# Kernel optimization log

Measured on AMD Instinct MI355X. Metric: run time of the kernel, lower is better.

The kernel has to match this reference:

```python
import jax, jax.numpy as jnp
import numpy as np

EMB_DIM, D_H, BSZ, SEQ = 2048, 128, 4, 4096
HALF = D_H // 2


def apply_rope(x, sin, cos):
    # x: [b, s, d]; sin/cos: [s, d//2]; interleaved-pair rotation
    b, s, d = x.shape
    xr = x.reshape(b, s, d // 2, 2)
    x0, x1 = xr[..., 0], xr[..., 1]
    r0 = x0 * cos - x1 * sin
    r1 = x1 * cos + x0 * sin
    return jnp.stack([r0, r1], axis=-1).reshape(b, s, d)


def setup_inputs() -> dict:
    key = jax.random.key(0)
    kx, kq, kk, kv = jax.random.split(key, 4)
    x = jax.random.normal(kx, (BSZ, SEQ, EMB_DIM), dtype=jnp.float32)
    # causal mask (1 = attend, 0 = masked), matching mask[q,:] slicing in source
    mask = jnp.tril(jnp.ones((SEQ, SEQ), dtype=jnp.int32))
    # standard RoPE angle tables: [seq, d_h//2]
    inv_freq = 1.0 / (10000.0 ** (jnp.arange(HALF, dtype=jnp.float32) / HALF))
    angles = jnp.arange(SEQ, dtype=jnp.float32)[:, None] * inv_freq[None, :]
    sin, cos = jnp.sin(angles), jnp.cos(angles)
    scale = 1.0 / np.sqrt(EMB_DIM)
    W_Q = jax.random.normal(kq, (EMB_DIM, D_H), dtype=jnp.float32) * scale
    W_K = jax.random.normal(kk, (EMB_DIM, D_H), dtype=jnp.float32) * scale
    W_V = jax.random.normal(kv, (EMB_DIM, D_H), dtype=jnp.float32) * scale
    return {"x": x, "mask": mask, "sin": sin, "cos": cos,
            "W_Q": W_Q, "W_K": W_K, "W_V": W_V}


def reference(x, mask, sin, cos, W_Q, W_V, W_K):
    # QKV projections
    Q = apply_rope(x @ W_Q, sin, cos)  # [b, s, d_h]
    K = apply_rope(x @ W_K, sin, cos)  # [b, s, d_h]
    V = x @ W_V                        # [b, s, d_h]
    # The source's chunked loop is exactly full masked attention over all K/V.
    scores = jnp.einsum('bqd,bkd->bqk', Q, K) / jnp.sqrt(jnp.float32(D_H))
    scores = jnp.where(mask[None, :, :] == 0, -jnp.inf, scores)
    attn = jax.nn.softmax(scores, axis=-1)
    return jnp.einsum('bqk,bkd->bqd', attn, V)
```

## Files before the change

### kernel.cpp

```cpp
#include <hip/hip_runtime.h>
#include <stdint.h>
#include <stddef.h>

typedef __bf16 bf16;
typedef __bf16 bf16x8 __attribute__((ext_vector_type(8)));
typedef float f32x4 __attribute__((ext_vector_type(4)));
typedef unsigned int uint32x2 __attribute__((ext_vector_type(2)));
typedef unsigned int uint32x4 __attribute__((ext_vector_type(4)));

typedef const __attribute__((address_space(1))) uint32_t GU32;
typedef __attribute__((address_space(3))) uint32_t LU32;

__device__ __forceinline__ f32x4 mfma16(bf16x8 a, bf16x8 b, f32x4 c) {
  return __builtin_amdgcn_mfma_f32_16x16x32_bf16(a, b, c, 0, 0, 0);
}
__device__ __forceinline__ void gload16(const void* g, void* l) {
  __builtin_amdgcn_global_load_lds((GU32*)g, (LU32*)l, 16, 0, 0);
}

__global__ __launch_bounds__(256) void k_prep(const float* __restrict__ Wq,
                                              const float* __restrict__ Wk,
                                              const float* __restrict__ Wv,
                                              bf16* __restrict__ Wct) {
  __shared__ float tile[64][65];
  const int tid = threadIdx.x;
  const int widx = blockIdx.x >> 6, rem = blockIdx.x & 63;
  const int k0 = (rem >> 1) * 64, n0 = (rem & 1) * 64;
  const float* W = (widx == 0) ? Wq : (widx == 1) ? Wk : Wv;
  const int rg = tid >> 4, cq = tid & 15;
#pragma unroll
  for (int i = 0; i < 4; ++i) {
    int krow = i * 16 + rg;
    f32x4 v = *(const f32x4*)(W + (size_t)(k0 + krow) * 128 + n0 + cq * 4);
#pragma unroll
    for (int j = 0; j < 4; ++j) tile[krow][cq * 4 + j] = v[j];
  }
  __syncthreads();
#pragma unroll
  for (int i = 0; i < 4; ++i) {
    int nrow = i * 16 + rg;
    union { bf16 h[4]; uint32x2 u; } pk;
#pragma unroll
    for (int j = 0; j < 4; ++j) pk.h[j] = (bf16)tile[cq * 4 + j][nrow];
    *(uint32x2*)(Wct + (size_t)(widx * 128 + n0 + nrow) * 2048 + k0 + cq * 4) = pk.u;
  }
}

__global__ __launch_bounds__(256, 2) void k_proj(
    const float* __restrict__ x, const float* __restrict__ sint, const float* __restrict__ cost,
    const bf16* __restrict__ Wct, bf16* __restrict__ Qg, bf16* __restrict__ Kg,
    bf16* __restrict__ Vtg) {
  __shared__ __align__(16) uint8_t smem[65536];
  const int tid = threadIdx.x;
  const int lane = tid & 63, w = tid >> 6;
  const int l15 = lane & 15, l16 = lane >> 4;
  const int logical = (blockIdx.x & 7) * 64 + (blockIdx.x >> 3);
  const int nb = logical & 1, mb = logical >> 1;
  const int wm = w >> 1, wn = w & 1;
  const int arow = tid >> 2, aj = tid & 3;

  f32x4 acc[2][6] = {};
  f32x4 regA[4], regB[4];

  const float* abase = x + (size_t)(mb * 64 + arow) * 2048 + aj * 16;

  auto stageB = [&](int buf, int ks) {
    uint8_t* bbm = smem + buf * 32768 + 8192;
    int k0 = ks * 64;
#pragma unroll
    for (int i = 0; i < 6; ++i) {
      int L = i * 4096 + tid * 16;
      int n = L >> 7, cp = (L >> 4) & 7;
      int cc = cp ^ (n & 7);
      const uint8_t* src = (const uint8_t*)Wct + (((size_t)(nb * 192 + n) * 2048 + k0 + cc * 8) << 1);
      gload16(src, bbm + i * 4096 + w * 1024);
    }
  };
  auto loadA = [&](int ks, f32x4* r) {
    const f32x4* p = (const f32x4*)(abase + ks * 64);
#pragma unroll
    for (int i = 0; i < 4; ++i) r[i] = p[i];
  };
  auto writeA = [&](int buf, const f32x4* r) {
    uint8_t* ab = smem + buf * 32768;
#pragma unroll
    for (int h = 0; h < 2; ++h) {
      union { bf16 v[8]; uint32x4 u; } pk;
#pragma unroll
      for (int e = 0; e < 8; ++e) pk.v[e] = (bf16)r[h * 2 + (e >> 2)][e & 3];
      int c = aj * 2 + h;
      *(uint32x4*)(ab + arow * 128 + (((c ^ (arow & 7)) & 7) << 4)) = pk.u;
    }
  };
  auto compute = [&](int buf) {
    uint8_t* ab = smem + buf * 32768;
    uint8_t* bbm = ab + 8192;
    bf16x8 af[2][2], bv[2][6];
#pragma unroll
    for (int kk = 0; kk < 2; ++kk) {
#pragma unroll
      for (int mt = 0; mt < 2; ++mt) {
        int ml = wm * 32 + mt * 16 + l15;
        af[kk][mt] = *(const bf16x8*)(ab + ml * 128 + (((kk * 4 + l16) ^ (ml & 7)) << 4));
      }
#pragma unroll
      for (int nt = 0; nt < 6; ++nt) {
        int nl = wn * 96 + nt * 16 + l15;
        bv[kk][nt] = *(const bf16x8*)(bbm + nl * 128 + (((kk * 4 + l16) ^ (nl & 7)) << 4));
      }
    }
    __builtin_amdgcn_s_setprio(1);
#pragma unroll
    for (int kk = 0; kk < 2; ++kk)
#pragma unroll
      for (int mt = 0; mt < 2; ++mt)
#pragma unroll
        for (int nt = 0; nt < 6; ++nt)
          acc[mt][nt] = mfma16(af[kk][mt], bv[kk][nt], acc[mt][nt]);
    __builtin_amdgcn_s_setprio(0);
  };

  loadA(0, regA);
  stageB(0, 0);
  loadA(1, regB);
  writeA(0, regA);
  asm volatile("s_waitcnt vmcnt(4)" ::: "memory");
  asm volatile("s_waitcnt lgkmcnt(0)" ::: "memory");
  __builtin_amdgcn_s_barrier();

  for (int ks = 0; ks < 30; ks += 2) {
    {
      stageB(1, ks + 1);
      loadA(ks + 2, regA);
      compute(0);
      writeA(1, regB);
      asm volatile("s_waitcnt vmcnt(4)" ::: "memory");
      asm volatile("s_waitcnt lgkmcnt(0)" ::: "memory");
      __builtin_amdgcn_s_barrier();
    }
    {
      stageB(0, ks + 2);
      loadA(ks + 3, regB);
      compute(1);
      writeA(0, regA);
      asm volatile("s_waitcnt vmcnt(4)" ::: "memory");
      asm volatile("s_waitcnt lgkmcnt(0)" ::: "memory");
      __builtin_amdgcn_s_barrier();
    }
  }
  {
    stageB(1, 31);
    compute(0);
    writeA(1, regB);
    asm volatile("s_waitcnt vmcnt(0)" ::: "memory");
    asm volatile("s_waitcnt lgkmcnt(0)" ::: "memory");
    __builtin_amdgcn_s_barrier();
  }
  compute(1);

#pragma unroll
  for (int mt = 0; mt < 2; ++mt) {
    int gm = mb * 64 + wm * 32 + mt * 16 + l16 * 4;
    int bb = gm >> 12, s0 = gm & 4095;
#pragma unroll
    for (int nt = 0; nt < 6; ++nt) {
      int jcol = nb * 192 + wn * 96 + nt * 16 + l15;
      f32x4 v = acc[mt][nt];
      if (jcol < 256) {
        int p = (jcol & 127) >> 1;
        bool even = ((jcol & 1) == 0);
#pragma unroll
        for (int r = 0; r < 4; ++r) {
          float pv = __shfl_xor(v[r], 1);
          int s = s0 + r;
          float cs = cost[s * 64 + p], sn = sint[s * 64 + p];
          float nv = even ? (v[r] * cs - pv * sn) : (v[r] * cs + pv * sn);
          bf16 hb = (bf16)nv;
          if (jcol < 128) Qg[((size_t)(bb << 12) + s) * 128 + jcol] = hb;
          else            Kg[((size_t)(bb << 12) + s) * 128 + jcol - 128] = hb;
        }
      } else {
        int d = jcol - 256;
        union { bf16 h[4]; uint32x2 u; } pk;
#pragma unroll
        for (int r = 0; r < 4; ++r) pk.h[r] = (bf16)v[r];
        *(uint32x2*)((uint8_t*)Vtg + (((size_t)(bb << 7) + d) * 4096 + s0) * 2) = pk.u;
      }
    }
  }
}

__global__ __launch_bounds__(256, 2) void k_attn(
    const bf16* __restrict__ Qg, const bf16* __restrict__ Kg, const bf16* __restrict__ Vtg,
    float* __restrict__ PO, float* __restrict__ ML) {
  __shared__ __align__(16) uint8_t smem[81920];
  const int tid = threadIdx.x;
  const int lane = tid & 63, w = tid >> 6;
  const int l15 = lane & 15, l16 = lane >> 4;

  int gid = blockIdx.x;
  int b = gid / 80, rr = gid % 80;
  int j, c;
  if (rr < 8)       { j = rr;                 c = 0; }
  else if (rr < 24) { j = 8 + ((rr - 8) >> 1);  c = (rr - 8) & 1; }
  else if (rr < 48) { j = 16 + (rr - 24) / 3;   c = (rr - 24) % 3; }
  else              { j = 24 + ((rr - 48) >> 2); c = (rr - 48) & 3; }

  const int q0w = j * 128 + w * 32;
  const int kv_lo = c * 1024;
  const int kv_hi = min((c + 1) * 1024, (j + 1) * 128);
  const int T = (kv_hi - kv_lo) >> 6;

  bf16x8 qf[2][4];
#pragma unroll
  for (int qt = 0; qt < 2; ++qt)
#pragma unroll
    for (int kk = 0; kk < 4; ++kk)
      qf[qt][kk] = *(const bf16x8*)(Qg + ((size_t)(b << 12) + q0w + qt * 16 + l15) * 128 + kk * 32 + l16 * 8);

  f32x4 o[2][8] = {};
  float m_r[2] = {-1e30f, -1e30f};
  float l_r[2] = {0.f, 0.f};
  uint8_t* pb = smem + 65536 + w * 4096;

  auto stage = [&](int t) {
    uint8_t* kb = smem + (t & 1) * 32768;
    uint8_t* vb = kb + 16384;
    int kv0 = kv_lo + t * 64;
#pragma unroll
    for (int i = 0; i < 4; ++i) {
      int L = i * 4096 + tid * 16;
      {
        int kv = L >> 8, cp = (L >> 4) & 15, cc = cp ^ (kv & 7);
        const uint8_t* src = (const uint8_t*)Kg + ((size_t)((b << 12) + kv0 + kv) << 8) + (cc << 4);
        gload16(src, kb + i * 4096 + w * 1024);
      }
      {
        int d = L >> 7, cp = (L >> 4) & 7, cc = cp ^ (d & 7);
        const uint8_t* src = (const uint8_t*)Vtg + ((size_t)(((b << 7) + d) << 12) + kv0 + (cc << 3)) * 2;
        gload16(src, vb + i * 4096 + w * 1024);
      }
    }
  };

  stage(0);
  __syncthreads();

  for (int t = 0; t < T; ++t) {
    if (t + 1 < T) stage(t + 1);
    const int kv0 = kv_lo + t * 64;
    if (kv0 <= q0w + 31) {
      uint8_t* kb = smem + (t & 1) * 32768;
      uint8_t* vb = kb + 16384;
      f32x4 sfr[4][2] = {};
#pragma unroll
      for (int kk = 0; kk < 4; ++kk) {
#pragma unroll
        for (int kvt = 0; kvt < 4; ++kvt) {
          int kvl = kvt * 16 + l15;
          bf16x8 kf = *(const bf16x8*)(kb + (kvl << 8) + (((kk * 4 + l16) ^ (kvl & 7)) << 4));
#pragma unroll
          for (int qt = 0; qt < 2; ++qt)
            sfr[kvt][qt] = mfma16(kf, qf[qt][kk], sfr[kvt][qt]);
        }
      }
      const bool need_mask = (kv0 + 63 > q0w);
      const float scale = 0.08838834764831845f;
#pragma unroll
      for (int qt = 0; qt < 2; ++qt) {
        const int q = q0w + qt * 16 + l15;
        float pvv[4][4];
        float tmax = -1e30f;
#pragma unroll
        for (int kvt = 0; kvt < 4; ++kvt)
#pragma unroll
          for (int r = 0; r < 4; ++r) {
            float sv = sfr[kvt][qt][r] * scale;
            if (need_mask) {
              int kv = kv0 + kvt * 16 + l16 * 4 + r;
              if (kv > q) sv = -1e30f;
            }
            pvv[kvt][r] = sv;
            tmax = fmaxf(tmax, sv);
          }
        tmax = fmaxf(tmax, __shfl_xor(tmax, 16));
        tmax = fmaxf(tmax, __shfl_xor(tmax, 32));
        float mnew = fmaxf(m_r[qt], tmax);
        float corr = __expf(m_r[qt] - mnew);
        m_r[qt] = mnew;
        float rs = 0.f;
#pragma unroll
        for (int kvt = 0; kvt < 4; ++kvt)
#pragma unroll
          for (int r = 0; r < 4; ++r) {
            float p = __expf(pvv[kvt][r] - mnew);
            pvv[kvt][r] = p;
            rs += p;
          }
        rs += __shfl_xor(rs, 16);
        rs += __shfl_xor(rs, 32);
        l_r[qt] = l_r[qt] * corr + rs;
        const int qrow = qt * 16 + l15;
#pragma unroll
        for (int kvt = 0; kvt < 4; ++kvt) {
          union { bf16 h[4]; uint32x2 u; } pk;
#pragma unroll
          for (int r = 0; r < 4; ++r) pk.h[r] = (bf16)pvv[kvt][r];
          int kv2 = kvt * 32 + l16 * 8;
          *(uint32x2*)(pb + qrow * 128 + ((((kv2 >> 4) ^ (qrow & 7)) << 4) | (kv2 & 15))) = pk.u;
        }
#pragma unroll
        for (int r = 0; r < 4; ++r) {
          float cr = __shfl(corr, l16 * 4 + r);
#pragma unroll
          for (int dt = 0; dt < 8; ++dt) o[qt][dt][r] *= cr;
        }
      }
#pragma unroll
      for (int kvb = 0; kvb < 2; ++kvb) {
        bf16x8 pa[2];
#pragma unroll
        for (int qt = 0; qt < 2; ++qt) {
          int qrow = qt * 16 + l15;
          int kv2 = kvb * 64 + l16 * 16;
          pa[qt] = *(const bf16x8*)(pb + qrow * 128 + (((kv2 >> 4) ^ (qrow & 7)) << 4));
        }
#pragma unroll
        for (int dt = 0; dt < 8; ++dt) {
          int d = dt * 16 + l15;
          bf16x8 vf = *(const bf16x8*)(vb + (d << 7) + (((kvb * 4 + l16) ^ (d & 7)) << 4));
#pragma unroll
          for (int qt = 0; qt < 2; ++qt)
            o[qt][dt] = mfma16(pa[qt], vf, o[qt][dt]);
        }
      }
    }
    __syncthreads();
  }

  float* POb = PO + (size_t)((b * 32 + j) * 4 + c) * 16384;
#pragma unroll
  for (int qt = 0; qt < 2; ++qt)
#pragma unroll
    for (int dt = 0; dt < 8; ++dt)
#pragma unroll
      for (int r = 0; r < 4; ++r)
        POb[(w * 32 + qt * 16 + l16 * 4 + r) * 128 + dt * 16 + l15] = o[qt][dt][r];
  float* MLb = ML + (size_t)((b * 32 + j) * 4 + c) * 256;
  if (l16 == 0) {
#pragma unroll
    for (int qt = 0; qt < 2; ++qt) {
      MLb[w * 32 + qt * 16 + l15] = m_r[qt];
      MLb[128 + w * 32 + qt * 16 + l15] = l_r[qt];
    }
  }
}

__global__ void k_combine(const float* __restrict__ PO, const float* __restrict__ ML,
                          float* __restrict__ out) {
  int blk = blockIdx.x;
  int b = blk >> 5, j = blk & 31;
  int nc = 1 + (j >> 3);
  int t = threadIdx.x;
  int q = t >> 1, half = t & 1;
  const float* MLb = ML + (size_t)(b * 32 + j) * 4 * 256;
  float mv[4], lv[4];
  float ms = -1e30f;
  for (int cc = 0; cc < nc; ++cc) {
    mv[cc] = MLb[cc * 256 + q];
    lv[cc] = MLb[cc * 256 + 128 + q];
    ms = fmaxf(ms, mv[cc]);
  }
  float wgt[4];
  float den = 0.f;
  for (int cc = 0; cc < nc; ++cc) { wgt[cc] = __expf(mv[cc] - ms); den += wgt[cc] * lv[cc]; }
  float inv = 1.f / den;
  const float* POb = PO + (size_t)(b * 32 + j) * 4 * 16384 + q * 128 + half * 64;
  float* ob = out + ((size_t)(b << 12) + j * 128 + q) * 128 + half * 64;
  for (int d = 0; d < 64; d += 4) {
    f32x4 a = {0.f, 0.f, 0.f, 0.f};
    for (int cc = 0; cc < nc; ++cc) {
      f32x4 v = *(const f32x4*)(POb + cc * 16384 + d);
      a += v * wgt[cc];
    }
    a *= inv;
    *(f32x4*)(ob + d) = a;
  }
}

extern "C" void kernel_launch(void* const* d_in, const int* in_sizes, int n_in,
                              void* d_out, int out_size, void* d_ws, size_t ws_size,
                              hipStream_t stream) {
  const float* x = (const float*)d_in[0];
  const float* sint = (const float*)d_in[2];
  const float* cost = (const float*)d_in[3];
  const float* Wq = (const float*)d_in[4];
  const float* Wk = (const float*)d_in[5];
  const float* Wv = (const float*)d_in[6];
  uint8_t* ws = (uint8_t*)d_ws;

  bf16* Wct = (bf16*)(ws + 0x0);
  bf16* Qg  = (bf16*)(ws + 0x180000);
  bf16* Kg  = (bf16*)(ws + 0x580000);
  bf16* Vtg = (bf16*)(ws + 0x980000);
  float* PO = (float*)(ws + 0xD80000);
  float* ML = (float*)(ws + 0x2D80000);
  float* out = (float*)d_out;

  hipLaunchKernelGGL(k_prep, dim3(192), dim3(256), 0, stream, Wq, Wk, Wv, Wct);
  hipLaunchKernelGGL(k_proj, dim3(512), dim3(256), 0, stream, x, sint, cost, Wct, Qg, Kg, Vtg);
  hipLaunchKernelGGL(k_attn, dim3(320), dim3(256), 0, stream, Qg, Kg, Vtg, PO, ML);
  hipLaunchKernelGGL(k_combine, dim3(128), dim3(256), 0, stream, PO, ML, out);
}
```

Before: 132.2 us.

## Give each projection block the full 384-column output so x is read once

The projection kernel now uses 512-thread blocks, each covering 64 rows across all 384 Q/K/V columns. Before, two blocks split the columns and each read and converted the same x tile. Each of the 8 waves owns 48 columns over all 64 rows, and LDS grows to 112 KB so only one block fits per CU. The aim is to halve the global reads of fp32 x, at the cost of fewer blocks (256), lower occupancy, and more B-tile LDS traffic per block.

```diff
diff --git a/kernel.cpp b/kernel.cpp
--- a/kernel.cpp
+++ b/kernel.cpp
@@ -46,66 +46,60 @@
   }
 }
 
-__global__ __launch_bounds__(256, 2) void k_proj(
+__global__ __launch_bounds__(512, 1) void k_proj(
     const float* __restrict__ x, const float* __restrict__ sint, const float* __restrict__ cost,
     const bf16* __restrict__ Wct, bf16* __restrict__ Qg, bf16* __restrict__ Kg,
     bf16* __restrict__ Vtg) {
-  __shared__ __align__(16) uint8_t smem[65536];
+  __shared__ __align__(16) uint8_t smem[114688];
   const int tid = threadIdx.x;
   const int lane = tid & 63, w = tid >> 6;
   const int l15 = lane & 15, l16 = lane >> 4;
-  const int logical = (blockIdx.x & 7) * 64 + (blockIdx.x >> 3);
-  const int nb = logical & 1, mb = logical >> 1;
-  const int wm = w >> 1, wn = w & 1;
-  const int arow = tid >> 2, aj = tid & 3;
-
-  f32x4 acc[2][6] = {};
-  f32x4 regA[4], regB[4];
-
-  const float* abase = x + (size_t)(mb * 64 + arow) * 2048 + aj * 16;
+  const int mb = blockIdx.x;
+  const int arow = tid >> 3, aj = tid & 7;
+
+  f32x4 acc[4][3] = {};
+  f32x4 regA[2], regB[2];
+
+  const float* abase = x + (size_t)(mb * 64 + arow) * 2048 + aj * 8;
 
   auto stageB = [&](int buf, int ks) {
-    uint8_t* bbm = smem + buf * 32768 + 8192;
+    uint8_t* bbm = smem + 16384 + buf * 49152;
     int k0 = ks * 64;
 #pragma unroll
     for (int i = 0; i < 6; ++i) {
-      int L = i * 4096 + tid * 16;
+      int L = i * 8192 + tid * 16;
       int n = L >> 7, cp = (L >> 4) & 7;
       int cc = cp ^ (n & 7);
-      const uint8_t* src = (const uint8_t*)Wct + (((size_t)(nb * 192 + n) * 2048 + k0 + cc * 8) << 1);
-      gload16(src, bbm + i * 4096 + w * 1024);
+      const uint8_t* src = (const uint8_t*)Wct + (((size_t)n * 2048 + k0 + cc * 8) << 1);
+      gload16(src, bbm + i * 8192 + w * 1024);
     }
   };
   auto loadA = [&](int ks, f32x4* r) {
     const f32x4* p = (const f32x4*)(abase + ks * 64);
-#pragma unroll
-    for (int i = 0; i < 4; ++i) r[i] = p[i];
+    r[0] = p[0];
+    r[1] = p[1];
   };
   auto writeA = [&](int buf, const f32x4* r) {
-    uint8_t* ab = smem + buf * 32768;
-#pragma unroll
-    for (int h = 0; h < 2; ++h) {
-      union { bf16 v[8]; uint32x4 u; } pk;
-#pragma unroll
-      for (int e = 0; e < 8; ++e) pk.v[e] = (bf16)r[h * 2 + (e >> 2)][e & 3];
-      int c = aj * 2 + h;
-      *(uint32x4*)(ab + arow * 128 + (((c ^ (arow & 7)) & 7) << 4)) = pk.u;
-    }
+    uint8_t* ab = smem + buf * 8192;
+    union { bf16 v[8]; uint32x4 u; } pk;
+#pragma unroll
+    for (int e = 0; e < 8; ++e) pk.v[e] = (bf16)r[e >> 2][e & 3];
+    *(uint32x4*)(ab + arow * 128 + (((aj ^ (arow & 7)) & 7) << 4)) = pk.u;
   };
   auto compute = [&](int buf) {
-    uint8_t* ab = smem + buf * 32768;
-    uint8_t* bbm = ab + 8192;
-    bf16x8 af[2][2], bv[2][6];
+    uint8_t* ab = smem + buf * 8192;
+    uint8_t* bbm = smem + 16384 + buf * 49152;
+    bf16x8 af[2][4], bv[2][3];
 #pragma unroll
     for (int kk = 0; kk < 2; ++kk) {
 #pragma unroll
-      for (int mt = 0; mt < 2; ++mt) {
-        int ml = wm * 32 + mt * 16 + l15;
+      for (int mt = 0; mt < 4; ++mt) {
+        int ml = mt * 16 + l15;
         af[kk][mt] = *(const bf16x8*)(ab + ml * 128 + (((kk * 4 + l16) ^ (ml & 7)) << 4));
       }
 #pragma unroll
-      for (int nt = 0; nt < 6; ++nt) {
-        int nl = wn * 96 + nt * 16 + l15;
+      for (int nt = 0; nt < 3; ++nt) {
+        int nl = w * 48 + nt * 16 + l15;
         bv[kk][nt] = *(const bf16x8*)(bbm + nl * 128 + (((kk * 4 + l16) ^ (nl & 7)) << 4));
       }
     }
@@ -113,9 +107,9 @@
 #pragma unroll
     for (int kk = 0; kk < 2; ++kk)
 #pragma unroll
-      for (int mt = 0; mt < 2; ++mt)
-#pragma unroll
-        for (int nt = 0; nt < 6; ++nt)
+      for (int mt = 0; mt < 4; ++mt)
+#pragma unroll
+        for (int nt = 0; nt < 3; ++nt)
           acc[mt][nt] = mfma16(af[kk][mt], bv[kk][nt], acc[mt][nt]);
     __builtin_amdgcn_s_setprio(0);
   };
@@ -124,7 +118,7 @@
   stageB(0, 0);
   loadA(1, regB);
   writeA(0, regA);
-  asm volatile("s_waitcnt vmcnt(4)" ::: "memory");
+  asm volatile("s_waitcnt vmcnt(2)" ::: "memory");
   asm volatile("s_waitcnt lgkmcnt(0)" ::: "memory");
   __builtin_amdgcn_s_barrier();
 
@@ -134,7 +128,7 @@
       loadA(ks + 2, regA);
       compute(0);
       writeA(1, regB);
-      asm volatile("s_waitcnt vmcnt(4)" ::: "memory");
+      asm volatile("s_waitcnt vmcnt(2)" ::: "memory");
       asm volatile("s_waitcnt lgkmcnt(0)" ::: "memory");
       __builtin_amdgcn_s_barrier();
     }
@@ -143,7 +137,7 @@
       loadA(ks + 3, regB);
       compute(1);
       writeA(0, regA);
-      asm volatile("s_waitcnt vmcnt(4)" ::: "memory");
+      asm volatile("s_waitcnt vmcnt(2)" ::: "memory");
       asm volatile("s_waitcnt lgkmcnt(0)" ::: "memory");
       __builtin_amdgcn_s_barrier();
     }
@@ -158,13 +152,14 @@
   }
   compute(1);
 
-#pragma unroll
-  for (int mt = 0; mt < 2; ++mt) {
-    int gm = mb * 64 + wm * 32 + mt * 16 + l16 * 4;
-    int bb = gm >> 12, s0 = gm & 4095;
-#pragma unroll
-    for (int nt = 0; nt < 6; ++nt) {
-      int jcol = nb * 192 + wn * 96 + nt * 16 + l15;
+  const int bb = mb >> 6;
+#pragma unroll
+  for (int mt = 0; mt < 4; ++mt) {
+    int gm = mb * 64 + mt * 16 + l16 * 4;
+    int s0 = gm & 4095;
+#pragma unroll
+    for (int nt = 0; nt < 3; ++nt) {
+      int jcol = w * 48 + nt * 16 + l15;
       f32x4 v = acc[mt][nt];
       if (jcol < 256) {
         int p = (jcol & 127) >> 1;
@@ -408,7 +403,7 @@
   float* out = (float*)d_out;
 
   hipLaunchKernelGGL(k_prep, dim3(192), dim3(256), 0, stream, Wq, Wk, Wv, Wct);
-  hipLaunchKernelGGL(k_proj, dim3(512), dim3(256), 0, stream, x, sint, cost, Wct, Qg, Kg, Vtg);
+  hipLaunchKernelGGL(k_proj, dim3(256), dim3(512), 0, stream, x, sint, cost, Wct, Qg, Kg, Vtg);
   hipLaunchKernelGGL(k_attn, dim3(320), dim3(256), 0, stream, Qg, Kg, Vtg, PO, ML);
   hipLaunchKernelGGL(k_combine, dim3(128), dim3(256), 0, stream, PO, ML, out);
 }
```

Measured after the change: 130.1 us. No clear change (-1.6%).
